# Performance work log

Measured on AMD Instinct MI355X. Metric: run time of the kernel, lower is better.

Reference implementation:

```python
import jax, jax.numpy as jnp
import numpy as np

DIM = 1024

def setup_inputs() -> dict:
    key = jax.random.key(0)
    k1, k2, k3, k4, k5 = jax.random.split(key, 5)
    B, Sq, Skv = 8, 2048, 2048
    x = jax.random.normal(k1, (B, Sq, DIM), dtype=jnp.float32)
    context = jax.random.normal(k2, (B, Skv, DIM), dtype=jnp.float32)
    # nn.Linear default init scale ~ uniform; use scaled normal for stability
    s = DIM ** -0.5
    Wq = jax.random.normal(k3, (DIM, DIM), dtype=jnp.float32) * s
    Wk = jax.random.normal(k4, (DIM, DIM), dtype=jnp.float32) * s
    Wv = jax.random.normal(k5, (DIM, DIM), dtype=jnp.float32) * s
    return {"x": x, "context": context, "Wq": Wq, "Wk": Wk, "Wv": Wv}

def reference(x, context, Wq, Wk, Wv):
    # Linear with weight W applied as x @ W.T (torch convention); here W is [out, in]
    q = jnp.einsum('bsd,ed->bse', x, Wq)          # [B, Sq, D]
    k = jnp.einsum('btd,ed->bte', context, Wk)    # [B, Skv, D]
    v = jnp.einsum('btd,ed->bte', context, Wv)    # [B, Skv, D]
    scale = Wq.shape[0] ** -0.5                   # dim ** -0.5 (no head split)
    dots = jnp.einsum('bse,bte->bst', q, k) * scale  # [B, Sq, Skv]
    attn = jax.nn.softmax(dots, axis=-1)
    out = jnp.einsum('bst,bte->bse', attn, v)     # [B, Sq, D]
    return out
```

## Files before the change

kernel.cpp:

```cpp
#include <hip/hip_runtime.h>


typedef unsigned short u16;
typedef __bf16 bf16x8 __attribute__((ext_vector_type(8)));
typedef float f32x4 __attribute__((ext_vector_type(4)));
typedef u16 us8 __attribute__((ext_vector_type(8)));

__device__ __forceinline__ u16 f2bf(float f) {
  unsigned int u = __float_as_uint(f);
  u += 0x7fffu + ((u >> 16) & 1u);
  return (u16)(u >> 16);
}
__device__ __forceinline__ float bf2f(u16 h) {
  return __uint_as_float((unsigned int)h << 16);
}

struct __attribute__((aligned(8))) us4 { u16 x, y, z, w; };

__global__ __launch_bounds__(256) void cvt_xc(const float4* __restrict__ x,
                                              const float4* __restrict__ c,
                                              us4* __restrict__ dx,
                                              us4* __restrict__ dc) {
  int i = blockIdx.x * 256 + threadIdx.x;
  const float4* s = (i < 4194304) ? x : (c - 4194304);
  us4* d = (i < 4194304) ? dx : (dc - 4194304);
  float4 v = s[i];
  us4 o{f2bf(v.x), f2bf(v.y), f2bf(v.z), f2bf(v.w)};
  d[i] = o;
}

__global__ __launch_bounds__(256) void cvt_w(const float4* __restrict__ wq,
                                             const float4* __restrict__ wk,
                                             const float4* __restrict__ wv,
                                             us4* __restrict__ d) {
  int i = blockIdx.x * 256 + threadIdx.x;
  const float4* s; float sc;
  if (i < 262144)      { s = wq;           sc = 0.03125f; }
  else if (i < 524288) { s = wk - 262144;  sc = 1.0f; }
  else                 { s = wv - 524288;  sc = 1.0f; }
  float4 v = s[i];
  us4 o{f2bf(v.x * sc), f2bf(v.y * sc), f2bf(v.z * sc), f2bf(v.w * sc)};
  d[i] = o;
}

__device__ __forceinline__ void gload16(const u16* g, u16* l) {
  __builtin_amdgcn_global_load_lds(
      (const __attribute__((address_space(1))) unsigned int*)g,
      (__attribute__((address_space(3))) unsigned int*)l,
      16, 0, 0);
}

template <bool BF16OUT>
__global__ __launch_bounds__(512, 2) void gemm_nt(
    const u16* __restrict__ A, const u16* __restrict__ B, void* __restrict__ Cout,
    int lda, int ldb, int ldc, int K,
    long batchA, long batchB, long batchC, int nx, int ny) {
  __shared__ u16 lds[65536];

  const int p    = blockIdx.x;
  const int slab = gridDim.x >> 3;
  const int gid  = (p & 7) * slab + (p >> 3);
  const int bx   = gid % nx;
  const int t2   = gid / nx;
  const int by   = t2 % ny;
  const int z    = t2 / ny;

  const int tid  = threadIdx.x;
  const int lane = tid & 63;
  const int wv   = tid >> 6;

  const u16* Ab = A + (size_t)z * batchA + (size_t)by * 256 * lda;
  const u16* Bb = B + (size_t)z * batchB + (size_t)bx * 256 * ldb;

  const int srow = tid >> 2;
  const int scol = ((tid & 3) ^ ((tid >> 3) & 3)) * 8;

  const u16* gA = Ab + (size_t)srow * lda + scol;
  const u16* gB = Bb + (size_t)srow * ldb + scol;
  const size_t a128 = (size_t)128 * lda, b128 = (size_t)128 * ldb;

  u16* dA = &lds[tid * 8];
  u16* dB = &lds[16384 + tid * 8];

  const int fr = lane & 15;
  const int xw = (((lane >> 4) ^ ((lane >> 1) & 3)) * 8);
  const int wm = (wv >> 2) * 128;
  const int wn = (wv & 3) * 64;
  const int rA = (wm + fr) * 32 + xw;
  const int rB = (wn + fr) * 32 + xw;

  const unsigned ldsb = (unsigned)(size_t)&lds[0];
  const unsigned bA0 = ldsb + (unsigned)(rA * 2);
  const unsigned bB0 = ldsb + 32768u + (unsigned)(rB * 2);

  f32x4 acc[8][4];
#pragma unroll
  for (int i = 0; i < 8; i++)
#pragma unroll
    for (int j = 0; j < 4; j++) acc[i][j] = (f32x4)0.f;

  const int NTt = K >> 6;

#define STAGE_A(BUF, KT, H) do {                                  \
    const u16* g_ = gA + (size_t)(KT) * 64 + (H) * 32;            \
    u16* d_ = dA + ((BUF) << 15) + (H) * 8192;                    \
    gload16(g_, d_); gload16(g_ + a128, d_ + 4096); } while (0)
#define STAGE_B(BUF, KT, H) do {                                  \
    const u16* g_ = gB + (size_t)(KT) * 64 + (H) * 32;            \
    u16* d_ = dB + ((BUF) << 15) + (H) * 8192;                    \
    gload16(g_, d_); gload16(g_ + b128, d_ + 4096); } while (0)
#define DSR(D, BASE, IMM)                                         \
    asm volatile("ds_read_b128 %0, %1 offset:" #IMM               \
                 : "=v"(D) : "v"(BASE))
#define LGKM(N) do {                                              \
    asm volatile("s_waitcnt lgkmcnt(" #N ")" ::: "memory");       \
    __builtin_amdgcn_sched_barrier(0); } while (0)
#define MFMA16(AR, AV, BV)                                        \
    __builtin_amdgcn_s_setprio(1);                                \
    _Pragma("unroll")                                             \
    for (int mi_ = 0; mi_ < 4; mi_++)                             \
      _Pragma("unroll")                                           \
      for (int ni_ = 0; ni_ < 4; ni_++)                           \
        acc[(AR) + mi_][ni_] = __builtin_amdgcn_mfma_f32_16x16x32_bf16( \
            __builtin_bit_cast(bf16x8, AV[mi_]),                  \
            __builtin_bit_cast(bf16x8, BV[ni_]),                  \
            acc[(AR) + mi_][ni_], 0, 0, 0);                       \
    __builtin_amdgcn_s_setprio(0);

  STAGE_A(0, 0, 0); STAGE_B(0, 0, 0); STAGE_A(0, 0, 1); STAGE_B(0, 0, 1);
  asm volatile("s_waitcnt vmcnt(0)" ::: "memory");
  __builtin_amdgcn_s_barrier();
  __builtin_amdgcn_sched_barrier(0);

  for (int kt = 0; kt < NTt; ++kt) {
    const unsigned bufo = (kt & 1) ? 65536u : 0u;
    const unsigned bA = bA0 + bufo;
    const unsigned bB = bB0 + bufo;
    const int nb = (kt & 1) ^ 1;
    const bool pf = (kt + 1 < NTt);
    f32x4 a0[4], a1[4], b0[4], c0[4], c1[4], d0[4];

    DSR(a0[0], bA, 0);     DSR(a0[1], bA, 1024);
    DSR(a0[2], bA, 2048);  DSR(a0[3], bA, 3072);
    DSR(b0[0], bB, 0);     DSR(b0[1], bB, 1024);
    DSR(b0[2], bB, 2048);  DSR(b0[3], bB, 3072);
    DSR(a1[0], bA, 4096);  DSR(a1[1], bA, 5120);
    DSR(a1[2], bA, 6144);  DSR(a1[3], bA, 7168);
    if (pf) { STAGE_A(nb, kt + 1, 0); STAGE_B(nb, kt + 1, 0);
              STAGE_A(nb, kt + 1, 1); STAGE_B(nb, kt + 1, 1); }

    LGKM(4);
    MFMA16(0, a0, b0)

    DSR(c0[0], bA, 16384); DSR(c0[1], bA, 17408);
    DSR(c0[2], bA, 18432); DSR(c0[3], bA, 19456);
    DSR(d0[0], bB, 16384); DSR(d0[1], bB, 17408);
    DSR(d0[2], bB, 18432); DSR(d0[3], bB, 19456);
    LGKM(8);
    MFMA16(4, a1, b0)

    DSR(c1[0], bA, 20480); DSR(c1[1], bA, 21504);
    DSR(c1[2], bA, 22528); DSR(c1[3], bA, 23552);
    LGKM(4);
    MFMA16(0, c0, d0)
    LGKM(0);
    MFMA16(4, c1, d0)

    if (pf) {
      asm volatile("s_waitcnt vmcnt(0)" ::: "memory");
      __builtin_amdgcn_s_barrier();
      __builtin_amdgcn_sched_barrier(0);
    }
  }

  const size_t cbase = (size_t)z * batchC;
  const int row0 = by * 256 + wm + (lane >> 4) * 4;
  const int col0 = bx * 256 + wn + fr;
#pragma unroll
  for (int mi = 0; mi < 8; mi++) {
#pragma unroll
    for (int i = 0; i < 4; i++) {
      const size_t roff = cbase + (size_t)(row0 + mi * 16 + i) * ldc + col0;
#pragma unroll
      for (int ni = 0; ni < 4; ni++) {
        float v = acc[mi][ni][i];
        if constexpr (BF16OUT)
          ((u16*)Cout)[roff + ni * 16] = f2bf(v);
        else
          ((float*)Cout)[roff + ni * 16] = v;
      }
    }
  }
#undef STAGE_A
#undef STAGE_B
#undef DSR
#undef LGKM
#undef MFMA16
}

__global__ __launch_bounds__(256) void softmax_rows_bf16(u16* __restrict__ SP) {
  const size_t row = blockIdx.x;
  us8* p = (us8*)(SP + row * 2048);
  const int t = threadIdx.x;
  us8 raw = p[t];
  float v[8];
#pragma unroll
  for (int i = 0; i < 8; i++) v[i] = bf2f(raw[i]);

  float m = v[0];
#pragma unroll
  for (int i = 1; i < 8; i++) m = fmaxf(m, v[i]);
#pragma unroll
  for (int o = 32; o; o >>= 1) m = fmaxf(m, __shfl_xor(m, o, 64));
  __shared__ float redm[4];
  if ((t & 63) == 0) redm[t >> 6] = m;
  __syncthreads();
  m = fmaxf(fmaxf(redm[0], redm[1]), fmaxf(redm[2], redm[3]));

  float sum = 0.f;
#pragma unroll
  for (int i = 0; i < 8; i++) { v[i] = __expf(v[i] - m); sum += v[i]; }
#pragma unroll
  for (int o = 32; o; o >>= 1) sum += __shfl_xor(sum, o, 64);
  __shared__ float reds[4];
  if ((t & 63) == 0) reds[t >> 6] = sum;
  __syncthreads();
  sum = reds[0] + reds[1] + reds[2] + reds[3];
  const float r = 1.0f / sum;

  us8 o;
#pragma unroll
  for (int i = 0; i < 8; i++) o[i] = f2bf(v[i] * r);
  p[t] = o;
}

extern "C" void kernel_launch(void* const* d_in, const int* in_sizes, int n_in,
                              void* d_out, int out_size, void* d_ws, size_t ws_size,
                              hipStream_t stream) {
  const float* x   = (const float*)d_in[0];
  const float* ctx = (const float*)d_in[1];
  const float* Wq  = (const float*)d_in[2];
  const float* Wk  = (const float*)d_in[3];
  const float* Wv  = (const float*)d_in[4];
  float* out = (float*)d_out;

  const size_t NT = 8ull * 2048 * 1024;

  u16* wsu  = (u16*)d_ws;
  u16* xbf  = wsu;
  u16* cbf  = wsu + NT;
  u16* Sbuf = wsu;
  u16* Vt   = wsu + 2 * NT;
  u16* Wqb  = wsu + 3 * NT;
  u16* Qbf = (u16*)d_out;

  dim3 blk(256), gblk(512);

  cvt_xc<<<dim3(32768), blk, 0, stream>>>((const float4*)x, (const float4*)ctx,
                                          (us4*)xbf, (us4*)cbf);
  cvt_w<<<dim3(3072), blk, 0, stream>>>((const float4*)Wq, (const float4*)Wk,
                                        (const float4*)Wv, (us4*)Wqb);

  gemm_nt<true><<<dim3(512), gblk, 0, stream>>>(
      xbf, Wqb, Qbf, 1024, 1024, 1024, 1024,
      (long)NT, 1024L * 1024, (long)NT, 4, 64);
  gemm_nt<true><<<dim3(256), gblk, 0, stream>>>(
      Wqb + 2 * 1024 * 1024, cbf, Vt, 1024, 1024, 2048, 1024,
      0L, 2048L * 1024, 1024L * 2048, 8, 4);

  gemm_nt<true><<<dim3(512), gblk, 0, stream>>>(
      Qbf, Qbf + NT, Sbuf, 1024, 1024, 2048, 1024,
      2048L * 1024, 2048L * 1024, 2048L * 2048, 8, 8);

  softmax_rows_bf16<<<dim3(16384), blk, 0, stream>>>(Sbuf);

  gemm_nt<false><<<dim3(256), gblk, 0, stream>>>(
      Sbuf, Vt, out, 2048, 2048, 1024, 2048,
      2048L * 2048, 1024L * 2048, 2048L * 1024, 4, 8);
}
```

Baseline: 429.1 us.

## Fuse softmax exp and normalization into the PV GEMM, merge conversion kernels

The softmax kernel no longer writes probabilities back. It only computes the per-row max and the reciprocal sum into a stats buffer. The final attn@V GEMM applies exp(s - max) to the score tile in LDS after each load and scales the accumulators by the reciprocal sum in the epilogue. This removes one full write pass over the 2048x2048 score matrix. The two fp32-to-bf16 conversion kernels are also merged into one launch. In exchange, the GEMM's K loop gets extra exp work and an LDS read-modify-write before each barrier, which lengthens the critical path of that GEMM.

```diff
diff --git a/kernel.cpp b/kernel.cpp
--- a/kernel.cpp
+++ b/kernel.cpp
@@ -17,30 +17,25 @@
 
 struct __attribute__((aligned(8))) us4 { u16 x, y, z, w; };
 
-__global__ __launch_bounds__(256) void cvt_xc(const float4* __restrict__ x,
-                                              const float4* __restrict__ c,
-                                              us4* __restrict__ dx,
-                                              us4* __restrict__ dc) {
+__global__ __launch_bounds__(256) void cvt_all(
+    const float4* __restrict__ x, const float4* __restrict__ c,
+    const float4* __restrict__ wq, const float4* __restrict__ wk,
+    const float4* __restrict__ wv,
+    us4* __restrict__ dxc, us4* __restrict__ dw) {
   int i = blockIdx.x * 256 + threadIdx.x;
-  const float4* s = (i < 4194304) ? x : (c - 4194304);
-  us4* d = (i < 4194304) ? dx : (dc - 4194304);
-  float4 v = s[i];
-  us4 o{f2bf(v.x), f2bf(v.y), f2bf(v.z), f2bf(v.w)};
-  d[i] = o;
-}
-
-__global__ __launch_bounds__(256) void cvt_w(const float4* __restrict__ wq,
-                                             const float4* __restrict__ wk,
-                                             const float4* __restrict__ wv,
-                                             us4* __restrict__ d) {
-  int i = blockIdx.x * 256 + threadIdx.x;
-  const float4* s; float sc;
-  if (i < 262144)      { s = wq;           sc = 0.03125f; }
-  else if (i < 524288) { s = wk - 262144;  sc = 1.0f; }
-  else                 { s = wv - 524288;  sc = 1.0f; }
-  float4 v = s[i];
+  const float4* s; us4* d; float sc = 1.0f;
+  if (i < 4194304)      { s = x + i;            d = dxc + i; }
+  else if (i < 8388608) { s = c + (i - 4194304); d = dxc + i; }
+  else {
+    int j = i - 8388608;
+    if (j < 262144)      { s = wq + j;            sc = 0.03125f; }
+    else if (j < 524288) { s = wk + (j - 262144); }
+    else                 { s = wv + (j - 524288); }
+    d = dw + j;
+  }
+  float4 v = *s;
   us4 o{f2bf(v.x * sc), f2bf(v.y * sc), f2bf(v.z * sc), f2bf(v.w * sc)};
-  d[i] = o;
+  *d = o;
 }
 
 __device__ __forceinline__ void gload16(const u16* g, u16* l) {
@@ -50,12 +45,14 @@
       16, 0, 0);
 }
 
-template <bool BF16OUT>
+template <bool BF16OUT, bool SM>
 __global__ __launch_bounds__(512, 2) void gemm_nt(
     const u16* __restrict__ A, const u16* __restrict__ B, void* __restrict__ Cout,
     int lda, int ldb, int ldc, int K,
-    long batchA, long batchB, long batchC, int nx, int ny) {
+    long batchA, long batchB, long batchC, int nx, int ny,
+    const float2* __restrict__ stats) {
   __shared__ u16 lds[65536];
+  __shared__ float rbuf[256];
 
   const int p    = blockIdx.x;
   const int slab = gridDim.x >> 3;
@@ -81,6 +78,14 @@
 
   u16* dA = &lds[tid * 8];
   u16* dB = &lds[16384 + tid * 8];
+
+  float mrow0 = 0.f, mrow1 = 0.f;
+  if constexpr (SM) {
+    const float2* st = stats + (size_t)z * 2048 + by * 256;
+    mrow0 = st[srow].x;
+    mrow1 = st[srow + 128].x;
+    if (tid < 256) rbuf[tid] = st[tid].y;
+  }
 
   const int fr = lane & 15;
   const int xw = (((lane >> 4) ^ ((lane >> 1) & 3)) * 8);
@@ -109,6 +114,20 @@
     const u16* g_ = gB + (size_t)(KT) * 64 + (H) * 32;            \
     u16* d_ = dB + ((BUF) << 15) + (H) * 8192;                    \
     gload16(g_, d_); gload16(g_ + b128, d_ + 4096); } while (0)
+#define XFORM(BUFO) do { if constexpr (SM) {                      \
+    u16* xb_ = dA + (BUFO);                                       \
+    _Pragma("unroll")                                             \
+    for (int s_ = 0; s_ < 4; s_++) {                              \
+      u16* p_ = xb_ + (s_ & 1) * 4096 + (s_ >> 1) * 8192;         \
+      const float mm_ = (s_ & 1) ? mrow1 : mrow0;                 \
+      us8 v_ = *(us8*)p_;                                         \
+      _Pragma("unroll")                                           \
+      for (int k_ = 0; k_ < 8; k_++)                              \
+        v_[k_] = f2bf(__expf(bf2f(v_[k_]) - mm_));                \
+      *(us8*)p_ = v_;                                             \
+    }                                                             \
+    asm volatile("s_waitcnt lgkmcnt(0)" ::: "memory");            \
+  } } while (0)
 #define DSR(D, BASE, IMM)                                         \
     asm volatile("ds_read_b128 %0, %1 offset:" #IMM               \
                  : "=v"(D) : "v"(BASE))
@@ -129,6 +148,7 @@
 
   STAGE_A(0, 0, 0); STAGE_B(0, 0, 0); STAGE_A(0, 0, 1); STAGE_B(0, 0, 1);
   asm volatile("s_waitcnt vmcnt(0)" ::: "memory");
+  XFORM(0);
   __builtin_amdgcn_s_barrier();
   __builtin_amdgcn_sched_barrier(0);
 
@@ -168,6 +188,7 @@
 
     if (pf) {
       asm volatile("s_waitcnt vmcnt(0)" ::: "memory");
+      XFORM((unsigned)nb << 15);
       __builtin_amdgcn_s_barrier();
       __builtin_amdgcn_sched_barrier(0);
     }
@@ -181,9 +202,12 @@
 #pragma unroll
     for (int i = 0; i < 4; i++) {
       const size_t roff = cbase + (size_t)(row0 + mi * 16 + i) * ldc + col0;
+      float rsc = 1.0f;
+      if constexpr (SM) rsc = rbuf[wm + (lane >> 4) * 4 + mi * 16 + i];
 #pragma unroll
       for (int ni = 0; ni < 4; ni++) {
         float v = acc[mi][ni][i];
+        if constexpr (SM) v *= rsc;
         if constexpr (BF16OUT)
           ((u16*)Cout)[roff + ni * 16] = f2bf(v);
         else
@@ -193,14 +217,16 @@
   }
 #undef STAGE_A
 #undef STAGE_B
+#undef XFORM
 #undef DSR
 #undef LGKM
 #undef MFMA16
 }
 
-__global__ __launch_bounds__(256) void softmax_rows_bf16(u16* __restrict__ SP) {
+__global__ __launch_bounds__(256) void row_stats_bf16(
+    const u16* __restrict__ SP, float2* __restrict__ st) {
   const size_t row = blockIdx.x;
-  us8* p = (us8*)(SP + row * 2048);
+  const us8* p = (const us8*)(SP + row * 2048);
   const int t = threadIdx.x;
   us8 raw = p[t];
   float v[8];
@@ -219,19 +245,16 @@
 
   float sum = 0.f;
 #pragma unroll
-  for (int i = 0; i < 8; i++) { v[i] = __expf(v[i] - m); sum += v[i]; }
+  for (int i = 0; i < 8; i++) sum += __expf(v[i] - m);
 #pragma unroll
   for (int o = 32; o; o >>= 1) sum += __shfl_xor(sum, o, 64);
   __shared__ float reds[4];
   if ((t & 63) == 0) reds[t >> 6] = sum;
   __syncthreads();
-  sum = reds[0] + reds[1] + reds[2] + reds[3];
-  const float r = 1.0f / sum;
-
-  us8 o;
-#pragma unroll
-  for (int i = 0; i < 8; i++) o[i] = f2bf(v[i] * r);
-  p[t] = o;
+  if (t == 0) {
+    sum = reds[0] + reds[1] + reds[2] + reds[3];
+    st[row] = make_float2(m, 1.0f / sum);
+  }
 }
 
 extern "C" void kernel_launch(void* const* d_in, const int* in_sizes, int n_in,
@@ -248,33 +271,32 @@
 
   u16* wsu  = (u16*)d_ws;
   u16* xbf  = wsu;
-  u16* cbf  = wsu + NT;
   u16* Sbuf = wsu;
   u16* Vt   = wsu + 2 * NT;
   u16* Wqb  = wsu + 3 * NT;
+  float2* stats = (float2*)Wqb;
   u16* Qbf = (u16*)d_out;
 
   dim3 blk(256), gblk(512);
 
-  cvt_xc<<<dim3(32768), blk, 0, stream>>>((const float4*)x, (const float4*)ctx,
-                                          (us4*)xbf, (us4*)cbf);
-  cvt_w<<<dim3(3072), blk, 0, stream>>>((const float4*)Wq, (const float4*)Wk,
-                                        (const float4*)Wv, (us4*)Wqb);
-
-  gemm_nt<true><<<dim3(512), gblk, 0, stream>>>(
+  cvt_all<<<dim3(35840), blk, 0, stream>>>(
+      (const float4*)x, (const float4*)ctx, (const float4*)Wq,
+      (const float4*)Wk, (const float4*)Wv, (us4*)xbf, (us4*)Wqb);
+
+  gemm_nt<true, false><<<dim3(512), gblk, 0, stream>>>(
       xbf, Wqb, Qbf, 1024, 1024, 1024, 1024,
-      (long)NT, 1024L * 1024, (long)NT, 4, 64);
-  gemm_nt<true><<<dim3(256), gblk, 0, stream>>>(
-      Wqb + 2 * 1024 * 1024, cbf, Vt, 1024, 1024, 2048, 1024,
-      0L, 2048L * 1024, 1024L * 2048, 8, 4);
-
-  gemm_nt<true><<<dim3(512), gblk, 0, stream>>>(
+      (long)NT, 1024L * 1024, (long)NT, 4, 64, nullptr);
+  gemm_nt<true, false><<<dim3(256), gblk, 0, stream>>>(
+      Wqb + 2 * 1024 * 1024, wsu + NT, Vt, 1024, 1024, 2048, 1024,
+      0L, 2048L * 1024, 1024L * 2048, 8, 4, nullptr);
+
+  gemm_nt<true, false><<<dim3(512), gblk, 0, stream>>>(
       Qbf, Qbf + NT, Sbuf, 1024, 1024, 2048, 1024,
-      2048L * 1024, 2048L * 1024, 2048L * 2048, 8, 8);
-
-  softmax_rows_bf16<<<dim3(16384), blk, 0, stream>>>(Sbuf);
-
-  gemm_nt<false><<<dim3(256), gblk, 0, stream>>>(
+      2048L * 1024, 2048L * 1024, 2048L * 2048, 8, 8, nullptr);
+
+  row_stats_bf16<<<dim3(16384), blk, 0, stream>>>(Sbuf, stats);
+
+  gemm_nt<false, true><<<dim3(256), gblk, 0, stream>>>(
       Sbuf, Vt, out, 2048, 2048, 1024, 2048,
-      2048L * 2048, 1024L * 2048, 2048L * 1024, 4, 8);
-}
+      2048L * 2048, 1024L * 2048, 2048L * 1024, 4, 8, stats);
+}
```

After: 436.0 us. No clear change (+1.6%).
